# Optimization experiments

Hardware: AMD Instinct MI355X
Metric: run time of the kernel (lower is better)

The kernel has to match this reference:

```python
import math
import jax, jax.numpy as jnp
import numpy as np

N_HEAD = 16
N_GROUPS = 32
EPS = 1e-05


def gelu(x):
    return 0.5 * x * (1.0 + jnp.tanh(math.sqrt(2.0 / math.pi) * (x + 0.044715 * x ** 3)))


def dp_group_norm(x, weight, bias, num_groups=N_GROUPS, eps=EPS):
    # x: [B, T, H]. torch F.group_norm on transposed [B, H, T] normalizes over
    # (channels_per_group, T) jointly per (batch, group).
    B, T, H = x.shape
    xg = x.reshape(B, T, num_groups, H // num_groups)
    mean = jnp.mean(xg, axis=(1, 3), keepdims=True)
    var = jnp.mean((xg - mean) ** 2, axis=(1, 3), keepdims=True)
    xn = ((xg - mean) / jnp.sqrt(var + eps)).reshape(B, T, H)
    return xn * weight + bias


def attention(x, w_attn, b_attn, w_aproj, b_aproj):
    B, T, H = x.shape
    hd = H // N_HEAD
    qkv = x @ w_attn + b_attn                      # [B, T, 3H]
    q, k, v = jnp.split(qkv, 3, axis=-1)
    q = q.reshape(B, T, N_HEAD, hd).transpose(0, 2, 1, 3)   # [B, nh, T, hd]
    k = k.reshape(B, T, N_HEAD, hd).transpose(0, 2, 1, 3)   # [B, nh, T, hd]
    v = v.reshape(B, T, N_HEAD, hd).transpose(0, 2, 1, 3)
    w = jnp.einsum('bhqd,bhkd->bhqk', q, k)        # no 1/sqrt(d): scale=False
    causal = jnp.tril(jnp.ones((T, T), dtype=x.dtype))
    w = w * causal - 1e10 * (1.0 - causal)
    w = jax.nn.softmax(w, axis=-1)
    a = jnp.einsum('bhqk,bhkd->bhqd', w, v)        # [B, nh, T, hd]
    a = a.transpose(0, 2, 1, 3).reshape(B, T, H)
    a = a @ w_aproj + b_aproj
    present = jnp.stack((k, v))                    # [2, B, nh, T, hd]
    return a, present


def setup_inputs() -> dict:
    key = jax.random.key(0)
    ks = jax.random.split(key, 6)
    B, T, H = 2, 2048, 1024
    return {
        'x': jax.random.normal(ks[0], (B, T, H), dtype=jnp.float32),
        'w_attn': jax.random.normal(ks[1], (H, 3 * H), dtype=jnp.float32) * 0.02,
        'b_attn': jnp.zeros((3 * H,), dtype=jnp.float32),
        'w_aproj': jax.random.normal(ks[2], (H, H), dtype=jnp.float32) * 0.02,
        'b_aproj': jnp.zeros((H,), dtype=jnp.float32),
        'ln1_w': jnp.ones((H,), dtype=jnp.float32),
        'ln1_b': jnp.zeros((H,), dtype=jnp.float32),
        'ln2_w': jnp.ones((H,), dtype=jnp.float32),
        'ln2_b': jnp.zeros((H,), dtype=jnp.float32),
        'w_fc': jax.random.normal(ks[3], (H, 4 * H), dtype=jnp.float32) * 0.02,
        'b_fc': jnp.zeros((4 * H,), dtype=jnp.float32),
        'w_mproj': jax.random.normal(ks[4], (4 * H, H), dtype=jnp.float32) * 0.02,
        'b_mproj': jnp.zeros((H,), dtype=jnp.float32),
    }


def reference(x, w_attn, b_attn, w_aproj, b_aproj, ln1_w, ln1_b, ln2_w, ln2_b,
              w_fc, b_fc, w_mproj, b_mproj):
    a, present = attention(dp_group_norm(x, ln1_w, ln1_b), w_attn, b_attn, w_aproj, b_aproj)
    x = x + a
    h = gelu(dp_group_norm(x, ln2_w, ln2_b) @ w_fc + b_fc)
    m = h @ w_mproj + b_mproj
    x = x + m
    return (x, present)
```

## Files before the change

kernel.cpp:

```cpp
#include <hip/hip_runtime.h>

#define B_  2
#define T_  2048
#define H_  1024
#define NH_ 16
#define HD_ 64
#define M_  (B_*T_)
#define PS_ 72

typedef __bf16 bf16x8 __attribute__((ext_vector_type(8)));
typedef float  floatx4 __attribute__((ext_vector_type(4)));

typedef __attribute__((address_space(1))) const unsigned int gas_u32;
typedef __attribute__((address_space(3))) unsigned int       las_u32;

__device__ __forceinline__ void gload_lds16(const __bf16* g, __bf16* l) {
    __builtin_amdgcn_global_load_lds((gas_u32*)g, (las_u32*)l, 16, 0, 0);
}

__global__ __launch_bounds__(256) void transpose_bf16(
    const float* __restrict__ in, __bf16* __restrict__ out, int K, int N)
{
    __shared__ float tile[32][33];
    const int k0 = blockIdx.x * 32, n0 = blockIdx.y * 32;
    const int tx = threadIdx.x & 31, ty = threadIdx.x >> 5;
#pragma unroll
    for (int i = 0; i < 32; i += 8)
        tile[ty + i][tx] = in[(size_t)(k0 + ty + i) * N + (n0 + tx)];
    __syncthreads();
#pragma unroll
    for (int i = 0; i < 32; i += 8)
        out[(size_t)(n0 + ty + i) * K + (k0 + tx)] = (__bf16)tile[tx][ty + i];
}

__global__ __launch_bounds__(256) void transpose_v(
    const __bf16* __restrict__ vb, __bf16* __restrict__ vtb)
{
    __shared__ __bf16 tile[32][33];
    const int bh = blockIdx.x;
    const int t0 = blockIdx.y * 32, d0 = blockIdx.z * 32;
    const __bf16* src = vb  + (size_t)bh * T_ * HD_;
    __bf16*       dst = vtb + (size_t)bh * HD_ * T_;
    const int tx = threadIdx.x & 31, ty = threadIdx.x >> 5;
#pragma unroll
    for (int i = 0; i < 32; i += 8)
        tile[ty + i][tx] = src[(size_t)(t0 + ty + i) * HD_ + (d0 + tx)];
    __syncthreads();
#pragma unroll
    for (int i = 0; i < 32; i += 8)
        dst[(size_t)(d0 + ty + i) * T_ + (t0 + tx)] = tile[tx][ty + i];
}

__global__ __launch_bounds__(256) void gn_partial(
    const float* __restrict__ x, float2* __restrict__ part)
{
    const int bg = blockIdx.x, chunk = blockIdx.y;
    const int batch = bg >> 5, g = bg & 31;
    const float* xp = x + (size_t)batch * T_ * H_ + g * 32;
    float s = 0.f, ss = 0.f;
    for (int i = threadIdx.x; i < 128 * 32; i += 256) {
        const int t = chunk * 128 + (i >> 5), c = i & 31;
        const float v = xp[(size_t)t * H_ + c];
        s += v; ss += v * v;
    }
#pragma unroll
    for (int off = 32; off > 0; off >>= 1) {
        s  += __shfl_down(s,  off, 64);
        ss += __shfl_down(ss, off, 64);
    }
    __shared__ float rs[4], rss[4];
    const int wv = threadIdx.x >> 6, lane = threadIdx.x & 63;
    if (lane == 0) { rs[wv] = s; rss[wv] = ss; }
    __syncthreads();
    if (threadIdx.x == 0)
        part[bg * 16 + chunk] =
            make_float2(rs[0] + rs[1] + rs[2] + rs[3],
                        rss[0] + rss[1] + rss[2] + rss[3]);
}

__global__ __launch_bounds__(64) void gn_finalize(
    const float2* __restrict__ part, float2* __restrict__ stats)
{
    const int bg = threadIdx.x;
    float s = 0.f, ss = 0.f;
#pragma unroll
    for (int i = 0; i < 16; ++i) {
        const float2 p = part[bg * 16 + i];
        s += p.x; ss += p.y;
    }
    const float inv = 1.f / (float)(T_ * 32);
    const float mean = s * inv;
    const float var  = ss * inv - mean * mean;
    stats[bg] = make_float2(mean, rsqrtf(var + 1e-5f));
}

__global__ __launch_bounds__(256) void gn_apply(
    const float* __restrict__ x, const float2* __restrict__ stats,
    const float* __restrict__ w, const float* __restrict__ bsc,
    __bf16* __restrict__ out)
{
    const size_t idx = ((size_t)blockIdx.x * 256 + threadIdx.x) * 4;
    const int h = (int)(idx & (H_ - 1));
    const int batch = (int)(idx >> 21);
    const float2 mr = stats[batch * 32 + (h >> 5)];
    const float4 xv = *(const float4*)(x + idx);
    const float4 wv = *(const float4*)(w + h);
    const float4 bv = *(const float4*)(bsc + h);
    __bf16 o[4];
    o[0] = (__bf16)((xv.x - mr.x) * mr.y * wv.x + bv.x);
    o[1] = (__bf16)((xv.y - mr.x) * mr.y * wv.y + bv.y);
    o[2] = (__bf16)((xv.z - mr.x) * mr.y * wv.z + bv.z);
    o[3] = (__bf16)((xv.w - mr.x) * mr.y * wv.w + bv.w);
    *(uint2*)(out + idx) = *(uint2*)o;
}

__device__ __forceinline__ void gemm_core256(
    const __bf16* __restrict__ A, const __bf16* __restrict__ BT,
    int K, int m0, int n0, __bf16* Sb, floatx4 (&acc)[8][4])
{
    const int tid = threadIdx.x, lane = tid & 63, wid = tid >> 6;
    const int quad = lane >> 4, l16 = lane & 15;
    const int wm = (wid >> 2) * 128, wn = (wid & 3) * 64;
    const int r0 = tid >> 2, cbs = tid & 3;
    const int sc  = ((cbs ^ ((r0 >> 1) & 3)) * 8);
    const int xq8 = (quad ^ ((l16 >> 1) & 3)) * 8;

    const __bf16* Ag = A  + (size_t)(m0 + r0) * K + sc;
    const __bf16* Bg = BT + (size_t)(n0 + r0) * K + sc;

#define STG256(b, kt)  do {                                                   \
    gload_lds16(Ag + (kt),                  Sb + (b)*16384 + tid*8);          \
    gload_lds16(Ag + (size_t)128*K + (kt),  Sb + (b)*16384 + 4096 + tid*8);   \
    gload_lds16(Bg + (kt),                  Sb + (b)*16384 + 8192 + tid*8);   \
    gload_lds16(Bg + (size_t)128*K + (kt),  Sb + (b)*16384 + 12288 + tid*8); } while (0)

    const int NT = K >> 5;
    STG256(0, 0);
    STG256(1, 32);
    STG256(2, 64);
    int cur = 0;
    for (int j = 0; j < NT; ++j) {
        const int kt = j << 5;
        if (j + 3 < NT) {
            STG256((cur + 3) & 3, kt + 96);
            asm volatile("s_waitcnt vmcnt(12)" ::: "memory");
        } else if (j + 2 < NT) {
            asm volatile("s_waitcnt vmcnt(8)" ::: "memory");
        } else if (j + 1 < NT) {
            asm volatile("s_waitcnt vmcnt(4)" ::: "memory");
        } else {
            asm volatile("s_waitcnt vmcnt(0)" ::: "memory");
        }
        __builtin_amdgcn_s_barrier();
        __builtin_amdgcn_sched_barrier(0);
        const __bf16* Ab = Sb + cur * 16384;
        const __bf16* Bb = Sb + cur * 16384 + 8192;
        bf16x8 af[8], bfg[4];
#pragma unroll
        for (int i = 0; i < 8; ++i)
            af[i]  = *(const bf16x8*)(Ab + (wm + i * 16 + l16) * 32 + xq8);
#pragma unroll
        for (int i = 0; i < 4; ++i)
            bfg[i] = *(const bf16x8*)(Bb + (wn + i * 16 + l16) * 32 + xq8);
        __builtin_amdgcn_s_setprio(1);
#pragma unroll
        for (int mi = 0; mi < 8; ++mi)
#pragma unroll
            for (int ni = 0; ni < 4; ++ni)
                acc[mi][ni] = __builtin_amdgcn_mfma_f32_16x16x32_bf16(
                    af[mi], bfg[ni], acc[mi][ni], 0, 0, 0);
        __builtin_amdgcn_s_setprio(0);
        __builtin_amdgcn_sched_barrier(0);
        __builtin_amdgcn_s_barrier();
        __builtin_amdgcn_sched_barrier(0);
        cur = (cur + 1) & 3;
    }
#undef STG256
}

#define GEMM256_PROLOGUE(KVAL)                                          \
    __shared__ __align__(16) __bf16 Sb[4 * 16384];          \
    const int m0 = blockIdx.x * 256, n0 = blockIdx.y * 256;             \
    floatx4 acc[8][4];                                                  \
    { floatx4 z = {0.f, 0.f, 0.f, 0.f};                                 \
      for (int i = 0; i < 8; ++i) for (int j = 0; j < 4; ++j) acc[i][j] = z; } \
    gemm_core256(A, BT, (KVAL), m0, n0, Sb, acc);                       \
    const int tid = threadIdx.x, lane = tid & 63, wid = tid >> 6;       \
    const int quad = lane >> 4, l16 = lane & 15;                        \
    const int wm = (wid >> 2) * 128, wn = (wid & 3) * 64;               \
    (void)tid;

__global__ __launch_bounds__(512) void gemm_qkv(
    const __bf16* __restrict__ A, const __bf16* __restrict__ BT,
    const float* __restrict__ bias, __bf16* __restrict__ qb,
    __bf16* __restrict__ kb, __bf16* __restrict__ vb,
    float* __restrict__ present)
{
    GEMM256_PROLOGUE(H_)
#pragma unroll
    for (int ni = 0; ni < 4; ++ni) {
        const int col = n0 + wn + ni * 16 + l16;
        const float bv = bias[col];
        const int which = col >> 10, c = col & 1023, hh = c >> 6, d = c & 63;
#pragma unroll
        for (int mi = 0; mi < 8; ++mi)
#pragma unroll
            for (int r = 0; r < 4; ++r) {
                const int row = m0 + wm + mi * 16 + quad * 4 + r;
                const int bb = row >> 11, t = row & 2047;
                const float v = acc[mi][ni][r] + bv;
                const size_t idx = (((size_t)bb * NH_ + hh) * T_ + t) * HD_ + d;
                if (which == 0)      qb[idx] = (__bf16)(v * 1.4426950408889634f);
                else if (which == 1) { kb[idx] = (__bf16)v; present[idx] = v; }
                else { vb[idx] = (__bf16)v;
                       present[(size_t)B_ * NH_ * T_ * HD_ + idx] = v; }
            }
    }
}

__global__ __launch_bounds__(512) void gemm_gelu(
    const __bf16* __restrict__ A, const __bf16* __restrict__ BT,
    const float* __restrict__ bias, __bf16* __restrict__ out)
{
    GEMM256_PROLOGUE(H_)
#pragma unroll
    for (int ni = 0; ni < 4; ++ni) {
        const int col = n0 + wn + ni * 16 + l16;
        const float bv = bias[col];
#pragma unroll
        for (int mi = 0; mi < 8; ++mi)
#pragma unroll
            for (int r = 0; r < 4; ++r) {
                const int row = m0 + wm + mi * 16 + quad * 4 + r;
                const float v = acc[mi][ni][r] + bv;
                const float e = exp2f(-2.3022082f * (v + 0.044715f * v * v * v));
                float rcp;
                asm("v_rcp_f32 %0, %1" : "=v"(rcp) : "v"(1.f + e));
                out[(size_t)row * (4 * H_) + col] = (__bf16)(v * rcp);
            }
    }
}

__global__ __launch_bounds__(256) void gemm_resid_n64(
    const __bf16* __restrict__ A, const __bf16* __restrict__ BT,
    const float* __restrict__ bias, const float* __restrict__ resid,
    float* __restrict__ out, int K, int N)
{
    __shared__ __align__(16) __bf16 As[3 * 8192], Bs[3 * 4096];
    const int m0 = blockIdx.x * 128, n0 = blockIdx.y * 64;
    const int tid  = threadIdx.x;
    const int lane = tid & 63, wv = tid >> 6;
    const int quad = lane >> 4, l16 = lane & 15;
    const int wm = (wv >> 1) * 64, wn = (wv & 1) * 32;
    const int r0 = tid >> 2;
    const int scs = (((tid & 3) ^ ((r0 >> 1) & 3)) * 8);
    const int xq8 = (quad ^ ((l16 >> 1) & 3)) * 8;

    floatx4 acc[4][2];
    { floatx4 z = {0.f, 0.f, 0.f, 0.f};
#pragma unroll
      for (int i = 0; i < 4; ++i) { acc[i][0] = z; acc[i][1] = z; } }

    const __bf16* Ag = A  + (size_t)(m0 + r0) * K + scs;
    const __bf16* Bg = BT + (size_t)(n0 + r0) * K + scs;

#define STGR(b, kt)  do {                                                     \
    _Pragma("unroll")                                                         \
    for (int s = 0; s < 2; ++s) {                                             \
        gload_lds16(Ag + (kt) + s * 32,                  As + (b)*8192 + s*4096 + tid*8);        \
        gload_lds16(Ag + (size_t)64 * K + (kt) + s * 32, As + (b)*8192 + s*4096 + 2048 + tid*8); \
        gload_lds16(Bg + (kt) + s * 32,                  Bs + (b)*4096 + s*2048 + tid*8);        \
    } } while (0)

    const int NT = K >> 6;
    STGR(0, 0);
    STGR(1, 64);
    int cur = 0;
    for (int j = 0; j < NT; ++j) {
        const int kt = j << 6;
        if (j + 2 < NT) {
            int nb = cur + 2; if (nb >= 3) nb -= 3;
            STGR(nb, kt + 128);
            asm volatile("s_waitcnt vmcnt(12)" ::: "memory");
        } else if (j + 1 < NT) {
            asm volatile("s_waitcnt vmcnt(6)" ::: "memory");
        } else {
            asm volatile("s_waitcnt vmcnt(0)" ::: "memory");
        }
        __builtin_amdgcn_s_barrier();
        __builtin_amdgcn_sched_barrier(0);
        const __bf16* Ab = As + cur * 8192;
        const __bf16* Bb = Bs + cur * 4096;
#pragma unroll
        for (int kk = 0; kk < 2; ++kk) {
            bf16x8 af[4], bfg[2];
#pragma unroll
            for (int i = 0; i < 4; ++i)
                af[i]  = *(const bf16x8*)(Ab + kk * 4096 + (wm + i * 16 + l16) * 32 + xq8);
#pragma unroll
            for (int i = 0; i < 2; ++i)
                bfg[i] = *(const bf16x8*)(Bb + kk * 2048 + (wn + i * 16 + l16) * 32 + xq8);
#pragma unroll
            for (int mi = 0; mi < 4; ++mi)
#pragma unroll
                for (int ni = 0; ni < 2; ++ni)
                    acc[mi][ni] = __builtin_amdgcn_mfma_f32_16x16x32_bf16(
                        af[mi], bfg[ni], acc[mi][ni], 0, 0, 0);
        }
        __builtin_amdgcn_sched_barrier(0);
        __builtin_amdgcn_s_barrier();
        __builtin_amdgcn_sched_barrier(0);
        cur = cur + 1; if (cur >= 3) cur = 0;
    }
#undef STGR

#pragma unroll
    for (int ni = 0; ni < 2; ++ni) {
        const int col = n0 + wn + ni * 16 + l16;
        const float bv = bias[col];
#pragma unroll
        for (int mi = 0; mi < 4; ++mi)
#pragma unroll
            for (int r = 0; r < 4; ++r) {
                const int row = m0 + wm + mi * 16 + quad * 4 + r;
                const size_t idx = (size_t)row * N + col;
                out[idx] = acc[mi][ni][r] + bv + resid[idx];
            }
    }
}

__global__ __launch_bounds__(256) void attn_kernel(
    const __bf16* __restrict__ qb, const __bf16* __restrict__ kb,
    const __bf16* __restrict__ vtb, __bf16* __restrict__ aout)
{
    const int bh = blockIdx.x;
    const int sp = 31 - blockIdx.y;
    const int bb = bh >> 4, hh = bh & 15;
    const __bf16* Q  = qb  + (size_t)bh * T_ * HD_;
    const __bf16* Kp = kb  + (size_t)bh * T_ * HD_;
    const __bf16* VT = vtb + (size_t)bh * HD_ * T_;
    __shared__ __align__(16) __bf16 Qs[2 * 2048];
    __shared__ __align__(16) __bf16 Ks[2][2 * 2048];
    __shared__ __align__(16) __bf16 Vs[2][2 * 2048];
    __shared__ __align__(16) __bf16 Ps[64 * PS_];

    const int tid = threadIdx.x, lane = tid & 63, wv = tid >> 6;
    const int quad = lane >> 4, l16 = lane & 15;
    const int sr = tid >> 2;
    const int scs = (((tid & 3) ^ ((sr >> 1) & 3)) * 8);
    const int xq8 = (quad ^ ((l16 >> 1) & 3)) * 8;

    const int q0 = sp * 64, nkt = sp + 1;

#pragma unroll
    for (int s = 0; s < 2; ++s) {
        gload_lds16(Q  + (size_t)(q0 + sr) * HD_ + s * 32 + scs, Qs + s * 2048 + tid * 8);
        gload_lds16(Kp + (size_t)sr * HD_ + s * 32 + scs, &Ks[0][s * 2048 + tid * 8]);
        gload_lds16(VT + (size_t)sr * T_  + s * 32 + scs, &Vs[0][s * 2048 + tid * 8]);
    }
    asm volatile("s_waitcnt vmcnt(0)" ::: "memory");
    __builtin_amdgcn_s_barrier();
    __builtin_amdgcn_sched_barrier(0);

    bf16x8 aq[2];
#pragma unroll
    for (int kk = 0; kk < 2; ++kk)
        aq[kk] = *(const bf16x8*)(Qs + kk * 2048 + (wv * 16 + l16) * 32 + xq8);

    float m_i[4], l_p[4];
    floatx4 Ov[4];
    { floatx4 z = {0.f, 0.f, 0.f, 0.f};
#pragma unroll
      for (int i = 0; i < 4; ++i) { Ov[i] = z; m_i[i] = -1e30f; l_p[i] = 0.f; } }

    int cur = 0;
    for (int kt = 0; kt < nkt; ++kt) {
        if (kt + 1 < nkt) {
            const int kn = (kt + 1) * 64;
#pragma unroll
            for (int s = 0; s < 2; ++s) {
                gload_lds16(Kp + (size_t)(kn + sr) * HD_ + s * 32 + scs,
                            &Ks[cur ^ 1][s * 2048 + tid * 8]);
                gload_lds16(VT + (size_t)sr * T_ + kn + s * 32 + scs,
                            &Vs[cur ^ 1][s * 2048 + tid * 8]);
            }
            asm volatile("s_waitcnt vmcnt(4)" ::: "memory");
        } else {
            asm volatile("s_waitcnt vmcnt(0)" ::: "memory");
        }
        __builtin_amdgcn_s_barrier();
        __builtin_amdgcn_sched_barrier(0);

        const __bf16* Kc = Ks[cur];
        const __bf16* Vc = Vs[cur];

        floatx4 sacc[4];
        { floatx4 z = {0.f, 0.f, 0.f, 0.f};
#pragma unroll
          for (int i = 0; i < 4; ++i) sacc[i] = z; }
#pragma unroll
        for (int kk = 0; kk < 2; ++kk)
#pragma unroll
            for (int ni = 0; ni < 4; ++ni) {
                const bf16x8 bk = *(const bf16x8*)(Kc + kk * 2048 + (ni * 16 + l16) * 32 + xq8);
                sacc[ni] = __builtin_amdgcn_mfma_f32_16x16x32_bf16(aq[kk], bk, sacc[ni], 0, 0, 0);
            }
        if (kt == sp) {
#pragma unroll
            for (int ni = 0; ni < 4; ++ni) {
                const int keyL = ni * 16 + l16;
#pragma unroll
                for (int r = 0; r < 4; ++r)
                    if (keyL > quad * 4 + r + wv * 16) sacc[ni][r] = -1e30f;
            }
        }
        float rmax[4];
#pragma unroll
        for (int r = 0; r < 4; ++r)
            rmax[r] = fmaxf(fmaxf(sacc[0][r], sacc[1][r]),
                            fmaxf(sacc[2][r], sacc[3][r]));
#pragma unroll
        for (int off = 1; off < 16; off <<= 1)
#pragma unroll
            for (int r = 0; r < 4; ++r)
                rmax[r] = fmaxf(rmax[r], __shfl_xor(rmax[r], off, 64));
        float need = rmax[0] - m_i[0];
#pragma unroll
        for (int r = 1; r < 4; ++r) need = fmaxf(need, rmax[r] - m_i[r]);
        if (__any(need > 8.f)) {
#pragma unroll
            for (int r = 0; r < 4; ++r) {
                const float mn = fmaxf(m_i[r], rmax[r]);
                const float al = exp2f(m_i[r] - mn);
                m_i[r] = mn;
                l_p[r] *= al;
#pragma unroll
                for (int ni = 0; ni < 4; ++ni) Ov[ni][r] *= al;
            }
        }
#pragma unroll
        for (int ni = 0; ni < 4; ++ni)
#pragma unroll
            for (int r = 0; r < 4; ++r) {
                const float pe = exp2f(sacc[ni][r] - m_i[r]);
                sacc[ni][r] = pe;
                l_p[r] += pe;
            }
#pragma unroll
        for (int ni = 0; ni < 4; ++ni)
#pragma unroll
            for (int r = 0; r < 4; ++r)
                Ps[(wv * 16 + quad * 4 + r) * PS_ + ni * 16 + l16] = (__bf16)sacc[ni][r];
#pragma unroll
        for (int kk = 0; kk < 2; ++kk) {
            const bf16x8 ap = *(const bf16x8*)(Ps + (wv * 16 + l16) * PS_ + kk * 32 + quad * 8);
#pragma unroll
            for (int ni = 0; ni < 4; ++ni) {
                const bf16x8 bv2 = *(const bf16x8*)(Vc + kk * 2048 + (ni * 16 + l16) * 32 + xq8);
                Ov[ni] = __builtin_amdgcn_mfma_f32_16x16x32_bf16(ap, bv2, Ov[ni], 0, 0, 0);
            }
        }
        __builtin_amdgcn_sched_barrier(0);
        __builtin_amdgcn_s_barrier();
        __builtin_amdgcn_sched_barrier(0);
        cur ^= 1;
    }
#pragma unroll
    for (int off = 1; off < 16; off <<= 1)
#pragma unroll
        for (int r = 0; r < 4; ++r)
            l_p[r] += __shfl_xor(l_p[r], off, 64);
#pragma unroll
    for (int ni = 0; ni < 4; ++ni)
#pragma unroll
        for (int r = 0; r < 4; ++r) {
            const int t = q0 + wv * 16 + quad * 4 + r;
            aout[((size_t)(bb * T_ + t)) * H_ + hh * HD_ + ni * 16 + l16] =
                (__bf16)(Ov[ni][r] / l_p[r]);
        }
}

extern "C" void kernel_launch(void* const* d_in, const int* in_sizes, int n_in,
                              void* d_out, int out_size, void* d_ws, size_t ws_size,
                              hipStream_t stream)
{
    (void)in_sizes; (void)n_in; (void)out_size; (void)ws_size;
    const float* x       = (const float*)d_in[0];
    const float* w_attn  = (const float*)d_in[1];
    const float* b_attn  = (const float*)d_in[2];
    const float* w_aproj = (const float*)d_in[3];
    const float* b_aproj = (const float*)d_in[4];
    const float* ln1_w   = (const float*)d_in[5];
    const float* ln1_b   = (const float*)d_in[6];
    const float* ln2_w   = (const float*)d_in[7];
    const float* ln2_b   = (const float*)d_in[8];
    const float* w_fc    = (const float*)d_in[9];
    const float* b_fc    = (const float*)d_in[10];
    const float* w_mproj = (const float*)d_in[11];
    const float* b_mproj = (const float*)d_in[12];
    float* out = (float*)d_out;
    float* present = out + (size_t)M_ * H_;

    char* wp = (char*)d_ws;
    auto alloc = [&](size_t bytes) {
        void* p = (void*)wp; wp += (bytes + 255) & ~(size_t)255; return p;
    };
    __bf16* A1       = (__bf16*)alloc((size_t)M_ * H_ * 2);
    __bf16* A2       = (__bf16*)alloc((size_t)M_ * H_ * 2);
    __bf16* WattnT   = (__bf16*)alloc((size_t)3 * H_ * H_ * 2);
    __bf16* WaprojT  = (__bf16*)alloc((size_t)H_ * H_ * 2);
    __bf16* WfcT     = (__bf16*)alloc((size_t)4 * H_ * H_ * 2);
    __bf16* WmprojT  = (__bf16*)alloc((size_t)4 * H_ * H_ * 2);
    __bf16* qb       = (__bf16*)alloc((size_t)M_ * H_ * 2);
    __bf16* kb       = (__bf16*)alloc((size_t)M_ * H_ * 2);
    __bf16* vb       = (__bf16*)alloc((size_t)M_ * H_ * 2);
    __bf16* vtb      = (__bf16*)alloc((size_t)M_ * H_ * 2);
    __bf16* attn_out = (__bf16*)alloc((size_t)M_ * H_ * 2);
    float*  x2       = (float*) alloc((size_t)M_ * H_ * 4);
    __bf16* Hbuf     = (__bf16*)alloc((size_t)M_ * 4 * H_ * 2);
    float2* gn_part  = (float2*)alloc(64 * 16 * sizeof(float2));
    float2* gn_stats = (float2*)alloc(64 * sizeof(float2));

    transpose_bf16<<<dim3(H_/32, 3*H_/32), 256, 0, stream>>>(w_attn,  WattnT,  H_,   3*H_);
    transpose_bf16<<<dim3(H_/32, H_/32),   256, 0, stream>>>(w_aproj, WaprojT, H_,   H_);
    transpose_bf16<<<dim3(H_/32, 4*H_/32), 256, 0, stream>>>(w_fc,    WfcT,    H_,   4*H_);
    transpose_bf16<<<dim3(4*H_/32, H_/32), 256, 0, stream>>>(w_mproj, WmprojT, 4*H_, H_);

    gn_partial <<<dim3(64, 16), 256, 0, stream>>>(x, gn_part);
    gn_finalize<<<1, 64, 0, stream>>>(gn_part, gn_stats);
    gn_apply   <<<M_*H_/1024, 256, 0, stream>>>(x, gn_stats, ln1_w, ln1_b, A1);

    gemm_qkv<<<dim3(M_/256, 3*H_/256), 512, 0, stream>>>(A1, WattnT, b_attn,
                                                         qb, kb, vb, present);
    transpose_v<<<dim3(B_*NH_, T_/32, HD_/32), 256, 0, stream>>>(vb, vtb);
    attn_kernel<<<dim3(32, 32), 256, 0, stream>>>(qb, kb, vtb, attn_out);
    gemm_resid_n64<<<dim3(M_/128, H_/64), 256, 0, stream>>>(attn_out, WaprojT, b_aproj,
                                                            x, x2, H_, H_);

    gn_partial <<<dim3(64, 16), 256, 0, stream>>>(x2, gn_part);
    gn_finalize<<<1, 64, 0, stream>>>(gn_part, gn_stats);
    gn_apply   <<<M_*H_/1024, 256, 0, stream>>>(x2, gn_stats, ln2_w, ln2_b, A2);

    gemm_gelu<<<dim3(M_/256, 4*H_/256), 512, 0, stream>>>(A2, WfcT, b_fc, Hbuf);
    gemm_resid_n64<<<dim3(M_/128, H_/64), 256, 0, stream>>>(Hbuf, WmprojT, b_mproj,
                                                            x2, out, 4*H_, H_);
}
```

Baseline: 407.9 us.

## Widen residual GEMM tile to 128x128 with BK=32 and defer attention row-max shuffles

The residual-add GEMM changes from a 128x64 tile with a K-step of 64 to a 128x128 tile with a K-step of 32. Each wave now computes a 64x64 sub-tile, which raises MFMA work per LDS fragment load, and s_setprio is raised around the MFMA block. The launch grid halves to 256 blocks, which may underfill the GPU's CUs and lowers parallelism. Separately, the attention kernel now does the cross-lane max-reduction shuffles only when a rescale is triggered, skipping the shuffle cost on most iterations.

```diff
diff --git a/kernel.cpp b/kernel.cpp
--- a/kernel.cpp
+++ b/kernel.cpp
@@ -241,81 +241,80 @@
     }
 }
 
-__global__ __launch_bounds__(256) void gemm_resid_n64(
+__global__ __launch_bounds__(256) void gemm_resid_128(
     const __bf16* __restrict__ A, const __bf16* __restrict__ BT,
     const float* __restrict__ bias, const float* __restrict__ resid,
     float* __restrict__ out, int K, int N)
 {
-    __shared__ __align__(16) __bf16 As[3 * 8192], Bs[3 * 4096];
-    const int m0 = blockIdx.x * 128, n0 = blockIdx.y * 64;
+    __shared__ __align__(16) __bf16 As[3 * 4096], Bs[3 * 4096];
+    const int m0 = blockIdx.x * 128, n0 = blockIdx.y * 128;
     const int tid  = threadIdx.x;
     const int lane = tid & 63, wv = tid >> 6;
     const int quad = lane >> 4, l16 = lane & 15;
-    const int wm = (wv >> 1) * 64, wn = (wv & 1) * 32;
+    const int wm = (wv >> 1) * 64, wn = (wv & 1) * 64;
     const int r0 = tid >> 2;
     const int scs = (((tid & 3) ^ ((r0 >> 1) & 3)) * 8);
     const int xq8 = (quad ^ ((l16 >> 1) & 3)) * 8;
 
-    floatx4 acc[4][2];
+    floatx4 acc[4][4];
     { floatx4 z = {0.f, 0.f, 0.f, 0.f};
 #pragma unroll
-      for (int i = 0; i < 4; ++i) { acc[i][0] = z; acc[i][1] = z; } }
+      for (int i = 0; i < 4; ++i)
+#pragma unroll
+          for (int j = 0; j < 4; ++j) acc[i][j] = z; }
 
     const __bf16* Ag = A  + (size_t)(m0 + r0) * K + scs;
     const __bf16* Bg = BT + (size_t)(n0 + r0) * K + scs;
 
-#define STGR(b, kt)  do {                                                     \
-    _Pragma("unroll")                                                         \
-    for (int s = 0; s < 2; ++s) {                                             \
-        gload_lds16(Ag + (kt) + s * 32,                  As + (b)*8192 + s*4096 + tid*8);        \
-        gload_lds16(Ag + (size_t)64 * K + (kt) + s * 32, As + (b)*8192 + s*4096 + 2048 + tid*8); \
-        gload_lds16(Bg + (kt) + s * 32,                  Bs + (b)*4096 + s*2048 + tid*8);        \
-    } } while (0)
-
-    const int NT = K >> 6;
-    STGR(0, 0);
-    STGR(1, 64);
+#define STGR3(b, kt)  do {                                                    \
+    gload_lds16(Ag + (kt),                  As + (b)*4096 + tid*8);           \
+    gload_lds16(Ag + (size_t)64 * K + (kt), As + (b)*4096 + 2048 + tid*8);    \
+    gload_lds16(Bg + (kt),                  Bs + (b)*4096 + tid*8);           \
+    gload_lds16(Bg + (size_t)64 * K + (kt), Bs + (b)*4096 + 2048 + tid*8); } while (0)
+
+    const int NT = K >> 5;
+    STGR3(0, 0);
+    STGR3(1, 32);
     int cur = 0;
     for (int j = 0; j < NT; ++j) {
-        const int kt = j << 6;
+        const int kt = j << 5;
         if (j + 2 < NT) {
             int nb = cur + 2; if (nb >= 3) nb -= 3;
-            STGR(nb, kt + 128);
-            asm volatile("s_waitcnt vmcnt(12)" ::: "memory");
+            STGR3(nb, kt + 64);
+            asm volatile("s_waitcnt vmcnt(8)" ::: "memory");
         } else if (j + 1 < NT) {
-            asm volatile("s_waitcnt vmcnt(6)" ::: "memory");
+            asm volatile("s_waitcnt vmcnt(4)" ::: "memory");
         } else {
             asm volatile("s_waitcnt vmcnt(0)" ::: "memory");
         }
         __builtin_amdgcn_s_barrier();
         __builtin_amdgcn_sched_barrier(0);
-        const __bf16* Ab = As + cur * 8192;
+        const __bf16* Ab = As + cur * 4096;
         const __bf16* Bb = Bs + cur * 4096;
-#pragma unroll
-        for (int kk = 0; kk < 2; ++kk) {
-            bf16x8 af[4], bfg[2];
-#pragma unroll
-            for (int i = 0; i < 4; ++i)
-                af[i]  = *(const bf16x8*)(Ab + kk * 4096 + (wm + i * 16 + l16) * 32 + xq8);
-#pragma unroll
-            for (int i = 0; i < 2; ++i)
-                bfg[i] = *(const bf16x8*)(Bb + kk * 2048 + (wn + i * 16 + l16) * 32 + xq8);
-#pragma unroll
-            for (int mi = 0; mi < 4; ++mi)
-#pragma unroll
-                for (int ni = 0; ni < 2; ++ni)
-                    acc[mi][ni] = __builtin_amdgcn_mfma_f32_16x16x32_bf16(
-                        af[mi], bfg[ni], acc[mi][ni], 0, 0, 0);
-        }
+        bf16x8 af[4], bfg[4];
+#pragma unroll
+        for (int i = 0; i < 4; ++i)
+            af[i]  = *(const bf16x8*)(Ab + (wm + i * 16 + l16) * 32 + xq8);
+#pragma unroll
+        for (int i = 0; i < 4; ++i)
+            bfg[i] = *(const bf16x8*)(Bb + (wn + i * 16 + l16) * 32 + xq8);
+        __builtin_amdgcn_s_setprio(1);
+#pragma unroll
+        for (int mi = 0; mi < 4; ++mi)
+#pragma unroll
+            for (int ni = 0; ni < 4; ++ni)
+                acc[mi][ni] = __builtin_amdgcn_mfma_f32_16x16x32_bf16(
+                    af[mi], bfg[ni], acc[mi][ni], 0, 0, 0);
+        __builtin_amdgcn_s_setprio(0);
         __builtin_amdgcn_sched_barrier(0);
         __builtin_amdgcn_s_barrier();
         __builtin_amdgcn_sched_barrier(0);
         cur = cur + 1; if (cur >= 3) cur = 0;
     }
-#undef STGR
-
-#pragma unroll
-    for (int ni = 0; ni < 2; ++ni) {
+#undef STGR3
+
+#pragma unroll
+    for (int ni = 0; ni < 4; ++ni) {
         const int col = n0 + wn + ni * 16 + l16;
         const float bv = bias[col];
 #pragma unroll
@@ -414,23 +413,23 @@
                     if (keyL > quad * 4 + r + wv * 16) sacc[ni][r] = -1e30f;
             }
         }
-        float rmax[4];
+        float rml[4];
 #pragma unroll
         for (int r = 0; r < 4; ++r)
-            rmax[r] = fmaxf(fmaxf(sacc[0][r], sacc[1][r]),
-                            fmaxf(sacc[2][r], sacc[3][r]));
-#pragma unroll
-        for (int off = 1; off < 16; off <<= 1)
-#pragma unroll
-            for (int r = 0; r < 4; ++r)
-                rmax[r] = fmaxf(rmax[r], __shfl_xor(rmax[r], off, 64));
-        float need = rmax[0] - m_i[0];
-#pragma unroll
-        for (int r = 1; r < 4; ++r) need = fmaxf(need, rmax[r] - m_i[r]);
+            rml[r] = fmaxf(fmaxf(sacc[0][r], sacc[1][r]),
+                           fmaxf(sacc[2][r], sacc[3][r]));
+        float need = rml[0] - m_i[0];
+#pragma unroll
+        for (int r = 1; r < 4; ++r) need = fmaxf(need, rml[r] - m_i[r]);
         if (__any(need > 8.f)) {
 #pragma unroll
+            for (int off = 1; off < 16; off <<= 1)
+#pragma unroll
+                for (int r = 0; r < 4; ++r)
+                    rml[r] = fmaxf(rml[r], __shfl_xor(rml[r], off, 64));
+#pragma unroll
             for (int r = 0; r < 4; ++r) {
-                const float mn = fmaxf(m_i[r], rmax[r]);
+                const float mn = fmaxf(m_i[r], rml[r]);
                 const float al = exp2f(m_i[r] - mn);
                 m_i[r] = mn;
                 l_p[r] *= al;
@@ -534,14 +533,14 @@
                                                          qb, kb, vb, present);
     transpose_v<<<dim3(B_*NH_, T_/32, HD_/32), 256, 0, stream>>>(vb, vtb);
     attn_kernel<<<dim3(32, 32), 256, 0, stream>>>(qb, kb, vtb, attn_out);
-    gemm_resid_n64<<<dim3(M_/128, H_/64), 256, 0, stream>>>(attn_out, WaprojT, b_aproj,
-                                                            x, x2, H_, H_);
+    gemm_resid_128<<<dim3(M_/128, H_/128), 256, 0, stream>>>(attn_out, WaprojT, b_aproj,
+                                                             x, x2, H_, H_);
 
     gn_partial <<<dim3(64, 16), 256, 0, stream>>>(x2, gn_part);
     gn_finalize<<<1, 64, 0, stream>>>(gn_part, gn_stats);
     gn_apply   <<<M_*H_/1024, 256, 0, stream>>>(x2, gn_stats, ln2_w, ln2_b, A2);
 
     gemm_gelu<<<dim3(M_/256, 4*H_/256), 512, 0, stream>>>(A2, WfcT, b_fc, Hbuf);
-    gemm_resid_n64<<<dim3(M_/128, H_/64), 256, 0, stream>>>(Hbuf, WmprojT, b_mproj,
-                                                            x2, out, 4*H_, H_);
-}
+    gemm_resid_128<<<dim3(M_/128, H_/128), 256, 0, stream>>>(Hbuf, WmprojT, b_mproj,
+                                                             x2, out, 4*H_, H_);
+}
```

New measurement: 418.9 us. 1.03x slower.
